# Kernel tuning notes

Measured on AMD Instinct MI355X. Metric: run time of the kernel, lower is better.

Reference implementation:

```python
import jax, jax.numpy as jnp
import numpy as np

B, S, PLM, G = 8, 2048, 768, 256
N_WM, E_WM = 50000, 800000
N_F, E_F = B * S, 131072
K = 4


def _gnn(h, src, dst, Ws, bs, n_nodes):
    # simple GCN-style message passing: aggregate neighbor features via
    # gather (h[src]) + scatter-add (segment_sum), then linear + relu.
    for W, b in zip(Ws, bs):
        m = jax.ops.segment_sum(h[src], dst, num_segments=n_nodes)  # [n, g]
        h = jax.nn.relu((h + m) @ W + b)
    return h


def setup_inputs() -> dict:
    key = jax.random.key(0)
    ks = jax.random.split(key, 16)
    std = 0.02
    inp = {
        "text_embeddings": jax.random.normal(ks[0], (B, S, PLM), jnp.float32),
        "wm_x": jax.random.normal(ks[1], (N_WM, G), jnp.float32),
        "wm_edge_index": jax.random.randint(ks[2], (2, E_WM), 0, N_WM),
        "token2nodepos": jax.random.randint(ks[3], (B * S, K), 0, N_WM),
        "fstm_node_ids": jax.random.randint(ks[4], (N_F,), 0, N_F),
        "fstm_edge_index": jax.random.randint(ks[5], (2, E_F), 0, N_F),
        # extra_emb: nn.Embedding(2, G, padding_idx=0) -> row 0 is zeros
        "extra_emb": jax.random.normal(ks[6], (2, G), jnp.float32).at[0].set(0.0) * std,
        "wm_W1": jax.random.normal(ks[7], (G, G), jnp.float32) * std,
        "wm_b1": jnp.zeros((G,), jnp.float32),
        "wm_W2": jax.random.normal(ks[8], (G, G), jnp.float32) * std,
        "wm_b2": jnp.zeros((G,), jnp.float32),
        "fstm_W1": jax.random.normal(ks[9], (G, G), jnp.float32) * std,
        "fstm_b1": jnp.zeros((G,), jnp.float32),
        "fstm_W2": jax.random.normal(ks[10], (G, G), jnp.float32) * std,
        "fstm_b2": jnp.zeros((G,), jnp.float32),
        "fc1_W": jax.random.normal(ks[11], (G + PLM, G), jnp.float32) * std,
        "fc1_b": jnp.zeros((G,), jnp.float32),
        "fc3_W": jax.random.normal(ks[12], (PLM + 2 * G, PLM), jnp.float32) * std,
        "fc3_b": jnp.zeros((PLM,), jnp.float32),
    }
    return inp


def reference(text_embeddings, wm_x, wm_edge_index, token2nodepos, fstm_node_ids,
              fstm_edge_index, extra_emb, wm_W1, wm_b1, wm_W2, wm_b2,
              fstm_W1, fstm_b1, fstm_W2, fstm_b2, fc1_W, fc1_b, fc3_W, fc3_b):
    # ====== WM ======
    graph_embeddings = _gnn(wm_x, wm_edge_index[0], wm_edge_index[1],
                            (wm_W1, wm_W2), (wm_b1, wm_b2), N_WM)  # [N_WM, G]
    table = jnp.concatenate([extra_emb, graph_embeddings], axis=0)  # [N_WM+2, G]
    # per-token gather-sum over K concept slots (original python loop, vectorized)
    tmp = jnp.sum(table[token2nodepos + 2], axis=1)  # [B*S, G]
    text_flat = text_embeddings.reshape(B * S, PLM)
    graph_text_embed = jnp.concatenate([tmp, text_flat], axis=-1) @ fc1_W + fc1_b  # [B*S, G]
    # ====== FSTM ======
    x = graph_text_embed[fstm_node_ids]  # [B*S, G]
    temporal = _gnn(x, fstm_edge_index[0], fstm_edge_index[1],
                    (fstm_W1, fstm_W2), (fstm_b1, fstm_b2), N_F)
    temporal = temporal.reshape(B, S, G)
    # ====== Final ======
    final_vec = jnp.concatenate(
        [text_embeddings, tmp.reshape(B, S, G), temporal], axis=-1)
    logits = final_vec @ fc3_W + fc3_b  # [B, S, PLM]
    return logits
```

## Files before the change

kernel.cpp:

```cpp
#include <hip/hip_runtime.h>

#define Bsz 8
#define Ssz 2048
#define PLM 768
#define Gd  256
#define N_WM 50000
#define E_WM 800000
#define N_F  16384
#define E_F  131072
#define Kc   4

typedef unsigned short ushort_t;
typedef short short8 __attribute__((ext_vector_type(8)));
typedef float f32x4 __attribute__((ext_vector_type(4)));

__device__ __forceinline__ ushort_t f2bf(float f) {
    union { float f; unsigned int u; } v; v.f = f;
    unsigned int r = (v.u + 0x7fffu + ((v.u >> 16) & 1u)) >> 16;
    return (ushort_t)r;
}
__device__ __forceinline__ float bf2f(ushort_t b) {
    union { unsigned int u; float f; } v; v.u = ((unsigned int)b) << 16;
    return v.f;
}
__device__ __forceinline__ float4 bf4f(ushort4 u) {
    return make_float4(bf2f(u.x), bf2f(u.y), bf2f(u.z), bf2f(u.w));
}

__device__ __forceinline__ void gl2lds16(const ushort_t* g, ushort_t* l) {
    __builtin_amdgcn_global_load_lds(
        (const __attribute__((address_space(1))) unsigned int*)g,
        (__attribute__((address_space(3))) unsigned int*)l, 16, 0, 0);
}

__device__ __forceinline__ void cvt4(const float* __restrict__ in,
                                     ushort_t* __restrict__ out, int i, int n4) {
    if (i < n4) {
        float4 v = ((const float4*)in)[i];
        ushort4 u;
        u.x = f2bf(v.x); u.y = f2bf(v.y); u.z = f2bf(v.z); u.w = f2bf(v.w);
        ((ushort4*)out)[i] = u;
    }
}
__device__ __forceinline__ void wtx(const float* __restrict__ W,
                                    ushort_t* __restrict__ Wt, int K, int N, int idx) {
    if (idx < N * K) {
        int n = idx / K, k = idx % K;
        Wt[idx] = f2bf(W[(size_t)k * N + n]);
    }
}

__global__ void conv_all(const float* __restrict__ wm_x, const float* __restrict__ text,
                         const float* __restrict__ extra,
                         const float* __restrict__ W1, const float* __restrict__ W2,
                         const float* __restrict__ W3, const float* __restrict__ W4,
                         const float* __restrict__ W5, const float* __restrict__ W6,
                         ushort_t* __restrict__ Xb, ushort_t* __restrict__ Tx,
                         ushort_t* __restrict__ Exb,
                         ushort_t* __restrict__ T1, ushort_t* __restrict__ T2,
                         ushort_t* __restrict__ T3, ushort_t* __restrict__ T4,
                         ushort_t* __restrict__ T5, ushort_t* __restrict__ T6) {
    int b = blockIdx.x, t = threadIdx.x;
    if (b < 12500) { cvt4(wm_x, Xb, b * 256 + t, 3200000); return; }
    b -= 12500;
    if (b < 12288) { cvt4(text, Tx, b * 256 + t, 3145728); return; }
    b -= 12288;
    if (b < 1) { cvt4(extra, Exb, t, 128); return; }
    b -= 1;
    if (b < 256) { wtx(W1, T1, 256, 256, b * 256 + t); return; }
    b -= 256;
    if (b < 256) { wtx(W2, T2, 256, 256, b * 256 + t); return; }
    b -= 256;
    if (b < 256) { wtx(W3, T3, 256, 256, b * 256 + t); return; }
    b -= 256;
    if (b < 256) { wtx(W4, T4, 256, 256, b * 256 + t); return; }
    b -= 256;
    if (b < 1024) { wtx(W5, T5, 1024, 256, b * 256 + t); return; }
    b -= 1024;
    wtx(W6, T6, 1280, 768, b * 256 + t);
}

#define WM_P 512
#define WM_CH 1563
#define WM_SHIFT 8
#define FS_P 128
#define FS_CH 1024
#define FS_SHIFT 6

__global__ __launch_bounds__(256) void csr_p1(const int* __restrict__ wm_dst,
                                              const int* __restrict__ f_dst,
                                              int* __restrict__ Cwm,
                                              int* __restrict__ Cfs) {
    __shared__ int hist[256];
    int b = blockIdx.x, t = threadIdx.x;
    hist[t] = 0; __syncthreads();
    if (b < WM_P) {
        int e0 = b * WM_CH, e1 = e0 + WM_CH; if (e1 > E_WM) e1 = E_WM;
        for (int e = e0 + t; e < e1; e += 256)
            atomicAdd(&hist[wm_dst[e] >> WM_SHIFT], 1);
        __syncthreads();
        Cwm[b * 256 + t] = hist[t];
    } else {
        int p = b - WM_P;
        int e0 = p * FS_CH, e1 = e0 + FS_CH;
        for (int e = e0 + t; e < e1; e += 256)
            atomicAdd(&hist[f_dst[e] >> FS_SHIFT], 1);
        __syncthreads();
        Cfs[p * 256 + t] = hist[t];
    }
}

__global__ __launch_bounds__(256) void csr_p2a(int* __restrict__ Cwm, int* __restrict__ BTwm,
                                               int* __restrict__ Cfs, int* __restrict__ BTfs) {
    __shared__ int sm[256];
    int b = blockIdx.x, t = threadIdx.x;
    int* C; int* BT; int P; int bk;
    if (b < 256) { C = Cwm; BT = BTwm; P = WM_P; bk = b; }
    else         { C = Cfs; BT = BTfs; P = FS_P; bk = b - 256; }
    int half = P >> 1;
    int v0 = 0, v1 = 0;
    if (t < half) { v0 = C[(2 * t) * 256 + bk]; v1 = C[(2 * t + 1) * 256 + bk]; }
    int s = v0 + v1;
    sm[t] = s; __syncthreads();
#pragma unroll
    for (int st = 1; st < 256; st <<= 1) {
        int x = (t >= st) ? sm[t - st] : 0;
        __syncthreads();
        sm[t] += x;
        __syncthreads();
    }
    int ex = sm[t] - s;
    if (t < half) {
        C[(2 * t) * 256 + bk] = ex;
        C[(2 * t + 1) * 256 + bk] = ex + v0;
    }
    if (t == 255) BT[bk] = sm[255];
}

__global__ __launch_bounds__(256) void csr_p2b(const int* __restrict__ BTwm,
                                               int* __restrict__ BSwm,
                                               const int* __restrict__ BTfs,
                                               int* __restrict__ BSfs) {
    __shared__ int sm[256];
    int t = threadIdx.x;
    const int* BT = blockIdx.x ? BTfs : BTwm;
    int* BS = blockIdx.x ? BSfs : BSwm;
    int E = blockIdx.x ? E_F : E_WM;
    int v = BT[t];
    sm[t] = v; __syncthreads();
#pragma unroll
    for (int st = 1; st < 256; st <<= 1) {
        int x = (t >= st) ? sm[t - st] : 0;
        __syncthreads();
        sm[t] += x;
        __syncthreads();
    }
    BS[t] = sm[t] - v;
    if (t == 255) BS[256] = E;
}

__global__ __launch_bounds__(256) void csr_p3(const int* __restrict__ wm_src,
                                              const int* __restrict__ wm_dst,
                                              const int* __restrict__ Cwm,
                                              const int* __restrict__ BSwm,
                                              int2* __restrict__ SEwm,
                                              const int* __restrict__ f_src,
                                              const int* __restrict__ f_dst,
                                              const int* __restrict__ Cfs,
                                              const int* __restrict__ BSfs,
                                              int2* __restrict__ SEfs) {
    __shared__ int cur[256];
    int b = blockIdx.x, t = threadIdx.x;
    if (b < WM_P) {
        cur[t] = Cwm[b * 256 + t] + BSwm[t];
        __syncthreads();
        int e0 = b * WM_CH, e1 = e0 + WM_CH; if (e1 > E_WM) e1 = E_WM;
        for (int e = e0 + t; e < e1; e += 256) {
            int d = wm_dst[e], s = wm_src[e];
            int pos = atomicAdd(&cur[d >> WM_SHIFT], 1);
            SEwm[pos] = make_int2(s, d);
        }
    } else {
        int p = b - WM_P;
        cur[t] = Cfs[p * 256 + t] + BSfs[t];
        __syncthreads();
        int e0 = p * FS_CH, e1 = e0 + FS_CH;
        for (int e = e0 + t; e < e1; e += 256) {
            int d = f_dst[e], s = f_src[e];
            int pos = atomicAdd(&cur[d >> FS_SHIFT], 1);
            SEfs[pos] = make_int2(s, d);
        }
    }
}

__global__ __launch_bounds__(256) void csr_p4(const int2* __restrict__ SEwm,
                                              const int* __restrict__ BSwm,
                                              int* __restrict__ wm_off,
                                              int* __restrict__ wm_bkt,
                                              const int2* __restrict__ SEfs,
                                              const int* __restrict__ BSfs,
                                              int* __restrict__ fs_off,
                                              int* __restrict__ fs_bkt) {
    __shared__ int cnt[256];
    __shared__ int sm[256];
    int ob = blockIdx.x, t = threadIdx.x;
    const int2* SE; const int* BS; int* off; int* bkt;
    int b, nb0, n, E, bw;
    if (ob < 256) { SE = SEwm; BS = BSwm; off = wm_off; bkt = wm_bkt;
                    b = ob; nb0 = b << WM_SHIFT; n = N_WM; E = E_WM; bw = 256; }
    else          { SE = SEfs; BS = BSfs; off = fs_off; bkt = fs_bkt;
                    b = ob - 256; nb0 = b << FS_SHIFT; n = N_F; E = E_F; bw = 64; }
    int e0 = BS[b], e1 = BS[b + 1];
    cnt[t] = 0; __syncthreads();
    for (int e = e0 + t; e < e1; e += 256)
        atomicAdd(&cnt[SE[e].y - nb0], 1);
    __syncthreads();
    int v = cnt[t];
    sm[t] = v; __syncthreads();
#pragma unroll
    for (int st = 1; st < 256; st <<= 1) {
        int x = (t >= st) ? sm[t - st] : 0;
        __syncthreads();
        sm[t] += x;
        __syncthreads();
    }
    int ex = sm[t] - v;
    if (t < bw && nb0 + t < n) off[nb0 + t] = e0 + ex;
    if (b == 0 && t == 0) off[n] = E;
    __syncthreads();
    cnt[t] = e0 + ex;
    __syncthreads();
    for (int e = e0 + t; e < e1; e += 256) {
        int2 sd = SE[e];
        int pos = atomicAdd(&cnt[sd.y - nb0], 1);
        bkt[pos] = sd.x;
    }
}

__global__ void aggregate_kernel(const ushort_t* __restrict__ h,
                                 const int* __restrict__ off,
                                 const int* __restrict__ bucket,
                                 ushort_t* __restrict__ hm, int n) {
    int i = blockIdx.x * 4 + (threadIdx.x >> 6);
    if (i >= n) return;
    int lane = threadIdx.x & 63;
    int s0 = off[i], s1 = off[i + 1];
    const ushort4* hp = (const ushort4*)h;
    float4 acc = bf4f(hp[(size_t)i * 64 + lane]);
    int j = s0;
    for (; j + 8 <= s1; j += 8) {
        int b0 = bucket[j + 0], b1 = bucket[j + 1];
        int b2 = bucket[j + 2], b3 = bucket[j + 3];
        int b4 = bucket[j + 4], b5 = bucket[j + 5];
        int b6 = bucket[j + 6], b7 = bucket[j + 7];
        ushort4 r0 = hp[(size_t)b0 * 64 + lane];
        ushort4 r1 = hp[(size_t)b1 * 64 + lane];
        ushort4 r2 = hp[(size_t)b2 * 64 + lane];
        ushort4 r3 = hp[(size_t)b3 * 64 + lane];
        ushort4 r4 = hp[(size_t)b4 * 64 + lane];
        ushort4 r5 = hp[(size_t)b5 * 64 + lane];
        ushort4 r6 = hp[(size_t)b6 * 64 + lane];
        ushort4 r7 = hp[(size_t)b7 * 64 + lane];
        float4 v0 = bf4f(r0), v1 = bf4f(r1), v2 = bf4f(r2), v3 = bf4f(r3);
        float4 v4 = bf4f(r4), v5 = bf4f(r5), v6 = bf4f(r6), v7 = bf4f(r7);
        acc.x += v0.x + v1.x + v2.x + v3.x + v4.x + v5.x + v6.x + v7.x;
        acc.y += v0.y + v1.y + v2.y + v3.y + v4.y + v5.y + v6.y + v7.y;
        acc.z += v0.z + v1.z + v2.z + v3.z + v4.z + v5.z + v6.z + v7.z;
        acc.w += v0.w + v1.w + v2.w + v3.w + v4.w + v5.w + v6.w + v7.w;
    }
    for (; j + 2 <= s1; j += 2) {
        int b0 = bucket[j + 0], b1 = bucket[j + 1];
        ushort4 r0 = hp[(size_t)b0 * 64 + lane];
        ushort4 r1 = hp[(size_t)b1 * 64 + lane];
        float4 v0 = bf4f(r0), v1 = bf4f(r1);
        acc.x += v0.x + v1.x; acc.y += v0.y + v1.y;
        acc.z += v0.z + v1.z; acc.w += v0.w + v1.w;
    }
    if (j < s1) {
        int b0 = bucket[j];
        float4 v0 = bf4f(hp[(size_t)b0 * 64 + lane]);
        acc.x += v0.x; acc.y += v0.y; acc.z += v0.z; acc.w += v0.w;
    }
    ushort4 u;
    u.x = f2bf(acc.x); u.y = f2bf(acc.y); u.z = f2bf(acc.z); u.w = f2bf(acc.w);
    ((ushort4*)hm)[(size_t)i * 64 + lane] = u;
}

__global__ void tmp_kernel(const ushort_t* __restrict__ gemb,
                           const ushort_t* __restrict__ extra,
                           const int* __restrict__ t2np,
                           ushort_t* __restrict__ D) {
    int i = blockIdx.x * 4 + (threadIdx.x >> 6);
    int lane = threadIdx.x & 63;
    float4 s = make_float4(0.f, 0.f, 0.f, 0.f);
#pragma unroll
    for (int k = 0; k < Kc; ++k) {
        int idx = t2np[i * Kc + k] + 2;
        const ushort4* row = (idx < 2) ? (const ushort4*)(extra + (size_t)idx * Gd)
                                       : (const ushort4*)(gemb + (size_t)(idx - 2) * Gd);
        float4 v = bf4f(row[lane]);
        s.x += v.x; s.y += v.y; s.z += v.z; s.w += v.w;
    }
    ushort4 u;
    u.x = f2bf(s.x); u.y = f2bf(s.y); u.z = f2bf(s.z); u.w = f2bf(s.w);
    ((ushort4*)D)[(size_t)i * 64 + lane] = u;
}

__global__ void gather_kernel(const ushort_t* __restrict__ Ein,
                              const int* __restrict__ ids,
                              ushort_t* __restrict__ F) {
    int i = blockIdx.x * 4 + (threadIdx.x >> 6);
    int lane = threadIdx.x & 63;
    ((ushort4*)F)[(size_t)i * 64 + lane] =
        ((const ushort4*)Ein)[(size_t)ids[i] * 64 + lane];
}

#define TBM 128
#define TBN 128
#define TBK 64

__device__ __forceinline__ void xcd_swizzle(int& bx, int& by) {
    int gx = gridDim.x;
    int nwg = gx * gridDim.y;
    int orig = by * gx + bx;
    int q = nwg >> 3, r = nwg & 7;
    int xcd = orig & 7, loc = orig >> 3;
    int wg = (xcd < r ? xcd * (q + 1) : r * (q + 1) + (xcd - r) * q) + loc;
    bx = wg % gx;
    by = wg / gx;
}

template <int MODE, int OUTBF>
__global__ __launch_bounds__(256) void mfma_gemm(
    const ushort_t* __restrict__ p0, const ushort_t* __restrict__ p1,
    const ushort_t* __restrict__ p2, const ushort_t* __restrict__ Wt,
    const float* __restrict__ bias, void* __restrict__ Cv,
    int M, int N, int K, int relu) {
    __shared__ ushort_t As[TBM * TBK];
    __shared__ ushort_t Bs[TBN * TBK];

    int tid  = threadIdx.x;
    int lane = tid & 63;
    int wave = tid >> 6;
    int wm = (wave >> 1) * 64, wn = (wave & 1) * 64;
    int bx = blockIdx.x, by = blockIdx.y;
    xcd_swizzle(bx, by);
    int row0 = by * TBM, col0 = bx * TBN;
    int l15 = lane & 15, l4 = lane >> 4;

    f32x4 acc[4][4];
#pragma unroll
    for (int i = 0; i < 4; ++i)
#pragma unroll
        for (int j = 0; j < 4; ++j)
            acc[i][j] = (f32x4){0.f, 0.f, 0.f, 0.f};

    for (int k0 = 0; k0 < K; k0 += TBK) {
#pragma unroll
        for (int it = 0; it < 4; ++it) {
            int eb = it * 2048 + wave * 512;
            int le = eb + lane * 8;
            int r  = le >> 6;
            int kl = le & 63;
            int grow = row0 + r; if (grow > M - 1) grow = M - 1;
            int gk = k0 + kl;
            const ushort_t* gp;
            if (MODE == 0)
                gp = p0 + (size_t)grow * K + gk;
            else if (MODE == 2)
                gp = (gk < 256) ? p0 + (size_t)grow * 256 + gk
                                : p1 + (size_t)grow * 768 + (gk - 256);
            else
                gp = (gk < 768) ? p0 + (size_t)grow * 768 + gk
                   : (gk < 1024) ? p1 + (size_t)grow * 256 + (gk - 768)
                                 : p2 + (size_t)grow * 256 + (gk - 1024);
            gl2lds16(gp, &As[eb]);
        }
#pragma unroll
        for (int it = 0; it < 4; ++it) {
            int eb = it * 2048 + wave * 512;
            int le = eb + lane * 8;
            int nl = le >> 6;
            int kl = le & 63;
            const ushort_t* gp = Wt + (size_t)(col0 + nl) * K + k0 + kl;
            gl2lds16(gp, &Bs[eb]);
        }
        __syncthreads();

#pragma unroll
        for (int ks = 0; ks < TBK; ks += 32) {
            short8 af[4], bfr[4];
#pragma unroll
            for (int mi = 0; mi < 4; ++mi)
                af[mi] = *(const short8*)&As[(wm + mi * 16 + l15) * TBK + ks + l4 * 8];
#pragma unroll
            for (int ni = 0; ni < 4; ++ni)
                bfr[ni] = *(const short8*)&Bs[(wn + ni * 16 + l15) * TBK + ks + l4 * 8];
#pragma unroll
            for (int mi = 0; mi < 4; ++mi)
#pragma unroll
                for (int ni = 0; ni < 4; ++ni)
                    acc[mi][ni] = __builtin_amdgcn_mfma_f32_16x16x32_bf16(
                        af[mi], bfr[ni], acc[mi][ni], 0, 0, 0);
        }
        __syncthreads();
    }

#pragma unroll
    for (int ni = 0; ni < 4; ++ni) {
        int c = col0 + wn + ni * 16 + l15;
        float bv = bias[c];
#pragma unroll
        for (int mi = 0; mi < 4; ++mi) {
#pragma unroll
            for (int r = 0; r < 4; ++r) {
                int rr = row0 + wm + mi * 16 + l4 * 4 + r;
                if (rr < M) {
                    float v = acc[mi][ni][r] + bv;
                    if (relu) v = fmaxf(v, 0.f);
                    if (OUTBF) ((ushort_t*)Cv)[(size_t)rr * N + c] = f2bf(v);
                    else       ((float*)Cv)[(size_t)rr * N + c] = v;
                }
            }
        }
    }
}

extern "C" void kernel_launch(void* const* d_in, const int* in_sizes, int n_in,
                              void* d_out, int out_size, void* d_ws, size_t ws_size,
                              hipStream_t stream) {
    const float* text    = (const float*)d_in[0];
    const float* wm_x    = (const float*)d_in[1];
    const int*   wm_ei   = (const int*)d_in[2];
    const int*   t2np    = (const int*)d_in[3];
    const int*   f_ids   = (const int*)d_in[4];
    const int*   f_ei    = (const int*)d_in[5];
    const float* extra   = (const float*)d_in[6];
    const float* wm_W1   = (const float*)d_in[7];
    const float* wm_b1   = (const float*)d_in[8];
    const float* wm_W2   = (const float*)d_in[9];
    const float* wm_b2   = (const float*)d_in[10];
    const float* fs_W1   = (const float*)d_in[11];
    const float* fs_b1   = (const float*)d_in[12];
    const float* fs_W2   = (const float*)d_in[13];
    const float* fs_b2   = (const float*)d_in[14];
    const float* fc1_W   = (const float*)d_in[15];
    const float* fc1_b   = (const float*)d_in[16];
    const float* fc3_W   = (const float*)d_in[17];
    const float* fc3_b   = (const float*)d_in[18];
    float* out = (float*)d_out;

    ushort_t* Xb  = (ushort_t*)d_ws;
    ushort_t* Ag  = Xb + 12800000;
    ushort_t* Gm  = Ag + 12800000;
    ushort_t* Tx  = Gm + 12800000;
    ushort_t* Dt  = Tx + 12582912;
    ushort_t* Ee  = Dt + 4194304;
    ushort_t* Wv  = Ee + 4194304;
    ushort_t* wt_wm1 = Wv;
    ushort_t* wt_wm2 = wt_wm1 + 65536;
    ushort_t* wt_fs1 = wt_wm2 + 65536;
    ushort_t* wt_fs2 = wt_fs1 + 65536;
    ushort_t* wt_fc1 = wt_fs2 + 65536;
    ushort_t* wt_fc3 = wt_fc1 + 262144;
    ushort_t* Exb    = wt_fc3 + 983040;
    int* wm_off = (int*)(Exb + 512);
    int* fs_off = wm_off + N_WM + 1;
    int* wm_bkt = fs_off + N_F + 1;
    int* fs_bkt = wm_bkt + E_WM;
    int2* SEwm = (int2*)Ag;
    int2* SEfs = SEwm + E_WM;
    int*  Cwm  = (int*)(SEfs + E_F);
    int*  Cfs  = Cwm + WM_P * 256;
    int*  BTwm = Cfs + FS_P * 256;
    int*  BTfs = BTwm + 256;
    int*  BSwm = BTfs + 256;
    int*  BSfs = BSwm + 257;

    ushort_t* h1 = Xb;
    ushort_t* F  = Gm;
    ushort_t* H  = Gm + 4194304;
    ushort_t* T  = Ee;

    const int* wm_src = wm_ei;
    const int* wm_dst = wm_ei + E_WM;
    const int* f_src  = f_ei;
    const int* f_dst  = f_ei + E_F;

    dim3 blk(256);
    dim3 gW(Gd / TBN, (N_WM + TBM - 1) / TBM);
    dim3 gF(Gd / TBN, N_F / TBM);
    dim3 gO(PLM / TBN, N_F / TBM);

    csr_p1<<<WM_P + FS_P, blk, 0, stream>>>(wm_dst, f_dst, Cwm, Cfs);
    csr_p2a<<<512, blk, 0, stream>>>(Cwm, BTwm, Cfs, BTfs);
    csr_p2b<<<2, blk, 0, stream>>>(BTwm, BSwm, BTfs, BSfs);
    csr_p3<<<WM_P + FS_P, blk, 0, stream>>>(wm_src, wm_dst, Cwm, BSwm, SEwm,
                                            f_src, f_dst, Cfs, BSfs, SEfs);
    csr_p4<<<512, blk, 0, stream>>>(SEwm, BSwm, wm_off, wm_bkt,
                                    SEfs, BSfs, fs_off, fs_bkt);

    conv_all<<<30677, blk, 0, stream>>>(wm_x, text, extra,
                                        wm_W1, wm_W2, fs_W1, fs_W2, fc1_W, fc3_W,
                                        Xb, Tx, Exb,
                                        wt_wm1, wt_wm2, wt_fs1, wt_fs2,
                                        wt_fc1, wt_fc3);

    aggregate_kernel<<<(N_WM + 3) / 4, blk, 0, stream>>>(Xb, wm_off, wm_bkt, Ag, N_WM);
    mfma_gemm<0, 1><<<gW, blk, 0, stream>>>(Ag, nullptr, nullptr, wt_wm1, wm_b1,
                                            h1, N_WM, Gd, Gd, 1);
    aggregate_kernel<<<(N_WM + 3) / 4, blk, 0, stream>>>(h1, wm_off, wm_bkt, Ag, N_WM);
    mfma_gemm<0, 1><<<gW, blk, 0, stream>>>(Ag, nullptr, nullptr, wt_wm2, wm_b2,
                                            Gm, N_WM, Gd, Gd, 1);
    tmp_kernel<<<N_F / 4, blk, 0, stream>>>(Gm, Exb, t2np, Dt);
    mfma_gemm<2, 1><<<gF, blk, 0, stream>>>(Dt, Tx, nullptr, wt_fc1, fc1_b,
                                            Ee, N_F, Gd, Gd + PLM, 0);
    gather_kernel<<<N_F / 4, blk, 0, stream>>>(Ee, f_ids, F);
    aggregate_kernel<<<N_F / 4, blk, 0, stream>>>(F, fs_off, fs_bkt, Ag, N_F);
    mfma_gemm<0, 1><<<gF, blk, 0, stream>>>(Ag, nullptr, nullptr, wt_fs1, fs_b1,
                                            H, N_F, Gd, Gd, 1);
    aggregate_kernel<<<N_F / 4, blk, 0, stream>>>(H, fs_off, fs_bkt, Ag, N_F);
    mfma_gemm<0, 1><<<gF, blk, 0, stream>>>(Ag, nullptr, nullptr, wt_fs2, fs_b2,
                                            T, N_F, Gd, Gd, 1);
    mfma_gemm<3, 0><<<gO, blk, 0, stream>>>(Tx, Dt, T, wt_fc3, fc3_b,
                                            out, N_F, PLM, PLM + 2 * Gd, 0);
}
```

Before: 556.0 us.

## Tile weight transposes via LDS, swizzle GEMM LDS, shrink tiles, deepen gather unroll

Weight transpose-and-convert now goes through a 64x64 shared-memory tile, so both the global reads and the writes are coalesced instead of strided. The GEMM is templated on block size and switches to 64x128 tiles, which doubles the number of blocks for the small-N GEMMs. It also XOR-swizzles the LDS column index to cut bank conflicts on fragment reads. The aggregation loop is unrolled to 16 independent gathers for more memory-level parallelism, at the cost of more registers and per-block reuse.

```diff
diff --git a/kernel.cpp b/kernel.cpp
--- a/kernel.cpp
+++ b/kernel.cpp
@@ -42,11 +42,26 @@
         ((ushort4*)out)[i] = u;
     }
 }
-__device__ __forceinline__ void wtx(const float* __restrict__ W,
-                                    ushort_t* __restrict__ Wt, int K, int N, int idx) {
-    if (idx < N * K) {
-        int n = idx / K, k = idx % K;
-        Wt[idx] = f2bf(W[(size_t)k * N + n]);
+
+__device__ __forceinline__ void wtx_tile(const float* __restrict__ W,
+                                         ushort_t* __restrict__ Wt,
+                                         int K, int N, int tile,
+                                         ushort_t (*sm)[65]) {
+    int kt = K >> 6;
+    int k0 = (tile % kt) << 6;
+    int n0 = (tile / kt) << 6;
+    int t = threadIdx.x;
+    int tr = t >> 6, tc = t & 63;
+#pragma unroll
+    for (int p = 0; p < 16; ++p) {
+        int k = p * 4 + tr;
+        sm[k][tc] = f2bf(W[(size_t)(k0 + k) * N + n0 + tc]);
+    }
+    __syncthreads();
+#pragma unroll
+    for (int p = 0; p < 16; ++p) {
+        int n = p * 4 + tr;
+        Wt[(size_t)(n0 + n) * K + k0 + tc] = sm[tc][n];
     }
 }
 
@@ -60,6 +75,7 @@
                          ushort_t* __restrict__ T1, ushort_t* __restrict__ T2,
                          ushort_t* __restrict__ T3, ushort_t* __restrict__ T4,
                          ushort_t* __restrict__ T5, ushort_t* __restrict__ T6) {
+    __shared__ ushort_t sm[64][65];
     int b = blockIdx.x, t = threadIdx.x;
     if (b < 12500) { cvt4(wm_x, Xb, b * 256 + t, 3200000); return; }
     b -= 12500;
@@ -67,17 +83,17 @@
     b -= 12288;
     if (b < 1) { cvt4(extra, Exb, t, 128); return; }
     b -= 1;
-    if (b < 256) { wtx(W1, T1, 256, 256, b * 256 + t); return; }
-    b -= 256;
-    if (b < 256) { wtx(W2, T2, 256, 256, b * 256 + t); return; }
-    b -= 256;
-    if (b < 256) { wtx(W3, T3, 256, 256, b * 256 + t); return; }
-    b -= 256;
-    if (b < 256) { wtx(W4, T4, 256, 256, b * 256 + t); return; }
-    b -= 256;
-    if (b < 1024) { wtx(W5, T5, 1024, 256, b * 256 + t); return; }
-    b -= 1024;
-    wtx(W6, T6, 1280, 768, b * 256 + t);
+    if (b < 16) { wtx_tile(W1, T1, 256, 256, b, sm); return; }
+    b -= 16;
+    if (b < 16) { wtx_tile(W2, T2, 256, 256, b, sm); return; }
+    b -= 16;
+    if (b < 16) { wtx_tile(W3, T3, 256, 256, b, sm); return; }
+    b -= 16;
+    if (b < 16) { wtx_tile(W4, T4, 256, 256, b, sm); return; }
+    b -= 16;
+    if (b < 64) { wtx_tile(W5, T5, 1024, 256, b, sm); return; }
+    b -= 64;
+    wtx_tile(W6, T6, 1280, 768, b, sm);
 }
 
 #define WM_P 512
@@ -248,38 +264,35 @@
     const ushort4* hp = (const ushort4*)h;
     float4 acc = bf4f(hp[(size_t)i * 64 + lane]);
     int j = s0;
-    for (; j + 8 <= s1; j += 8) {
-        int b0 = bucket[j + 0], b1 = bucket[j + 1];
-        int b2 = bucket[j + 2], b3 = bucket[j + 3];
-        int b4 = bucket[j + 4], b5 = bucket[j + 5];
-        int b6 = bucket[j + 6], b7 = bucket[j + 7];
-        ushort4 r0 = hp[(size_t)b0 * 64 + lane];
-        ushort4 r1 = hp[(size_t)b1 * 64 + lane];
-        ushort4 r2 = hp[(size_t)b2 * 64 + lane];
-        ushort4 r3 = hp[(size_t)b3 * 64 + lane];
-        ushort4 r4 = hp[(size_t)b4 * 64 + lane];
-        ushort4 r5 = hp[(size_t)b5 * 64 + lane];
-        ushort4 r6 = hp[(size_t)b6 * 64 + lane];
-        ushort4 r7 = hp[(size_t)b7 * 64 + lane];
-        float4 v0 = bf4f(r0), v1 = bf4f(r1), v2 = bf4f(r2), v3 = bf4f(r3);
-        float4 v4 = bf4f(r4), v5 = bf4f(r5), v6 = bf4f(r6), v7 = bf4f(r7);
-        acc.x += v0.x + v1.x + v2.x + v3.x + v4.x + v5.x + v6.x + v7.x;
-        acc.y += v0.y + v1.y + v2.y + v3.y + v4.y + v5.y + v6.y + v7.y;
-        acc.z += v0.z + v1.z + v2.z + v3.z + v4.z + v5.z + v6.z + v7.z;
-        acc.w += v0.w + v1.w + v2.w + v3.w + v4.w + v5.w + v6.w + v7.w;
-    }
-    for (; j + 2 <= s1; j += 2) {
-        int b0 = bucket[j + 0], b1 = bucket[j + 1];
-        ushort4 r0 = hp[(size_t)b0 * 64 + lane];
-        ushort4 r1 = hp[(size_t)b1 * 64 + lane];
-        float4 v0 = bf4f(r0), v1 = bf4f(r1);
-        acc.x += v0.x + v1.x; acc.y += v0.y + v1.y;
-        acc.z += v0.z + v1.z; acc.w += v0.w + v1.w;
-    }
-    if (j < s1) {
-        int b0 = bucket[j];
-        float4 v0 = bf4f(hp[(size_t)b0 * 64 + lane]);
-        acc.x += v0.x; acc.y += v0.y; acc.z += v0.z; acc.w += v0.w;
+    for (; j + 16 <= s1; j += 16) {
+        int bb[16];
+#pragma unroll
+        for (int q = 0; q < 16; ++q) bb[q] = bucket[j + q];
+        ushort4 rr[16];
+#pragma unroll
+        for (int q = 0; q < 16; ++q) rr[q] = hp[(size_t)bb[q] * 64 + lane];
+#pragma unroll
+        for (int q = 0; q < 16; ++q) {
+            float4 v = bf4f(rr[q]);
+            acc.x += v.x; acc.y += v.y; acc.z += v.z; acc.w += v.w;
+        }
+    }
+    for (; j + 4 <= s1; j += 4) {
+        int bb[4];
+#pragma unroll
+        for (int q = 0; q < 4; ++q) bb[q] = bucket[j + q];
+        ushort4 rr[4];
+#pragma unroll
+        for (int q = 0; q < 4; ++q) rr[q] = hp[(size_t)bb[q] * 64 + lane];
+#pragma unroll
+        for (int q = 0; q < 4; ++q) {
+            float4 v = bf4f(rr[q]);
+            acc.x += v.x; acc.y += v.y; acc.z += v.z; acc.w += v.w;
+        }
+    }
+    for (; j < s1; ++j) {
+        float4 v = bf4f(hp[(size_t)bucket[j] * 64 + lane]);
+        acc.x += v.x; acc.y += v.y; acc.z += v.z; acc.w += v.w;
     }
     ushort4 u;
     u.x = f2bf(acc.x); u.y = f2bf(acc.y); u.z = f2bf(acc.z); u.w = f2bf(acc.w);
@@ -315,9 +328,9 @@
         ((const ushort4*)Ein)[(size_t)ids[i] * 64 + lane];
 }
 
-#define TBM 128
-#define TBN 128
 #define TBK 64
+#define GBM 64
+#define GBN 128
 
 __device__ __forceinline__ void xcd_swizzle(int& bx, int& by) {
     int gx = gridDim.x;
@@ -330,38 +343,42 @@
     by = wg / gx;
 }
 
-template <int MODE, int OUTBF>
+template <int MODE, int OUTBF, int BM, int BN>
 __global__ __launch_bounds__(256) void mfma_gemm(
     const ushort_t* __restrict__ p0, const ushort_t* __restrict__ p1,
     const ushort_t* __restrict__ p2, const ushort_t* __restrict__ Wt,
     const float* __restrict__ bias, void* __restrict__ Cv,
     int M, int N, int K, int relu) {
-    __shared__ ushort_t As[TBM * TBK];
-    __shared__ ushort_t Bs[TBN * TBK];
+    constexpr int MR = BM / 32;
+    constexpr int NR = BN / 32;
+    constexpr int A_IT = (BM * TBK) / 2048;
+    constexpr int B_IT = (BN * TBK) / 2048;
+    __shared__ ushort_t As[BM * TBK];
+    __shared__ ushort_t Bs[BN * TBK];
 
     int tid  = threadIdx.x;
     int lane = tid & 63;
     int wave = tid >> 6;
-    int wm = (wave >> 1) * 64, wn = (wave & 1) * 64;
+    int wm = (wave >> 1) * (BM / 2), wn = (wave & 1) * (BN / 2);
     int bx = blockIdx.x, by = blockIdx.y;
     xcd_swizzle(bx, by);
-    int row0 = by * TBM, col0 = bx * TBN;
+    int row0 = by * BM, col0 = bx * BN;
     int l15 = lane & 15, l4 = lane >> 4;
 
-    f32x4 acc[4][4];
-#pragma unroll
-    for (int i = 0; i < 4; ++i)
-#pragma unroll
-        for (int j = 0; j < 4; ++j)
+    f32x4 acc[MR][NR];
+#pragma unroll
+    for (int i = 0; i < MR; ++i)
+#pragma unroll
+        for (int j = 0; j < NR; ++j)
             acc[i][j] = (f32x4){0.f, 0.f, 0.f, 0.f};
 
     for (int k0 = 0; k0 < K; k0 += TBK) {
 #pragma unroll
-        for (int it = 0; it < 4; ++it) {
+        for (int it = 0; it < A_IT; ++it) {
             int eb = it * 2048 + wave * 512;
             int le = eb + lane * 8;
             int r  = le >> 6;
-            int kl = le & 63;
+            int kl = (le ^ ((r & 7) << 3)) & 63;
             int grow = row0 + r; if (grow > M - 1) grow = M - 1;
             int gk = k0 + kl;
             const ushort_t* gp;
@@ -377,11 +394,11 @@
             gl2lds16(gp, &As[eb]);
         }
 #pragma unroll
-        for (int it = 0; it < 4; ++it) {
+        for (int it = 0; it < B_IT; ++it) {
             int eb = it * 2048 + wave * 512;
             int le = eb + lane * 8;
             int nl = le >> 6;
-            int kl = le & 63;
+            int kl = (le ^ ((nl & 7) << 3)) & 63;
             const ushort_t* gp = Wt + (size_t)(col0 + nl) * K + k0 + kl;
             gl2lds16(gp, &Bs[eb]);
         }
@@ -389,17 +406,23 @@
 
 #pragma unroll
         for (int ks = 0; ks < TBK; ks += 32) {
-            short8 af[4], bfr[4];
-#pragma unroll
-            for (int mi = 0; mi < 4; ++mi)
-                af[mi] = *(const short8*)&As[(wm + mi * 16 + l15) * TBK + ks + l4 * 8];
-#pragma unroll
-            for (int ni = 0; ni < 4; ++ni)
-                bfr[ni] = *(const short8*)&Bs[(wn + ni * 16 + l15) * TBK + ks + l4 * 8];
-#pragma unroll
-            for (int mi = 0; mi < 4; ++mi)
-#pragma unroll
-                for (int ni = 0; ni < 4; ++ni)
+            short8 af[MR], bfr[NR];
+#pragma unroll
+            for (int mi = 0; mi < MR; ++mi) {
+                int row = wm + mi * 16 + l15;
+                int col = (ks + l4 * 8) ^ ((row & 7) << 3);
+                af[mi] = *(const short8*)&As[row * TBK + col];
+            }
+#pragma unroll
+            for (int ni = 0; ni < NR; ++ni) {
+                int row = wn + ni * 16 + l15;
+                int col = (ks + l4 * 8) ^ ((row & 7) << 3);
+                bfr[ni] = *(const short8*)&Bs[row * TBK + col];
+            }
+#pragma unroll
+            for (int mi = 0; mi < MR; ++mi)
+#pragma unroll
+                for (int ni = 0; ni < NR; ++ni)
                     acc[mi][ni] = __builtin_amdgcn_mfma_f32_16x16x32_bf16(
                         af[mi], bfr[ni], acc[mi][ni], 0, 0, 0);
         }
@@ -407,11 +430,11 @@
     }
 
 #pragma unroll
-    for (int ni = 0; ni < 4; ++ni) {
+    for (int ni = 0; ni < NR; ++ni) {
         int c = col0 + wn + ni * 16 + l15;
         float bv = bias[c];
 #pragma unroll
-        for (int mi = 0; mi < 4; ++mi) {
+        for (int mi = 0; mi < MR; ++mi) {
 #pragma unroll
             for (int r = 0; r < 4; ++r) {
                 int rr = row0 + wm + mi * 16 + l4 * 4 + r;
@@ -488,9 +511,9 @@
     const int* f_dst  = f_ei + E_F;
 
     dim3 blk(256);
-    dim3 gW(Gd / TBN, (N_WM + TBM - 1) / TBM);
-    dim3 gF(Gd / TBN, N_F / TBM);
-    dim3 gO(PLM / TBN, N_F / TBM);
+    dim3 gW(Gd / GBN, (N_WM + GBM - 1) / GBM);
+    dim3 gF(Gd / GBN, N_F / GBM);
+    dim3 gO(PLM / GBN, N_F / GBM);
 
     csr_p1<<<WM_P + FS_P, blk, 0, stream>>>(wm_dst, f_dst, Cwm, Cfs);
     csr_p2a<<<512, blk, 0, stream>>>(Cwm, BTwm, Cfs, BTfs);
@@ -500,28 +523,28 @@
     csr_p4<<<512, blk, 0, stream>>>(SEwm, BSwm, wm_off, wm_bkt,
                                     SEfs, BSfs, fs_off, fs_bkt);
 
-    conv_all<<<30677, blk, 0, stream>>>(wm_x, text, extra,
+    conv_all<<<25157, blk, 0, stream>>>(wm_x, text, extra,
                                         wm_W1, wm_W2, fs_W1, fs_W2, fc1_W, fc3_W,
                                         Xb, Tx, Exb,
                                         wt_wm1, wt_wm2, wt_fs1, wt_fs2,
                                         wt_fc1, wt_fc3);
 
     aggregate_kernel<<<(N_WM + 3) / 4, blk, 0, stream>>>(Xb, wm_off, wm_bkt, Ag, N_WM);
-    mfma_gemm<0, 1><<<gW, blk, 0, stream>>>(Ag, nullptr, nullptr, wt_wm1, wm_b1,
-                                            h1, N_WM, Gd, Gd, 1);
+    mfma_gemm<0, 1, GBM, GBN><<<gW, blk, 0, stream>>>(Ag, nullptr, nullptr, wt_wm1,
+                                                      wm_b1, h1, N_WM, Gd, Gd, 1);
     aggregate_kernel<<<(N_WM + 3) / 4, blk, 0, stream>>>(h1, wm_off, wm_bkt, Ag, N_WM);
-    mfma_gemm<0, 1><<<gW, blk, 0, stream>>>(Ag, nullptr, nullptr, wt_wm2, wm_b2,
-                                            Gm, N_WM, Gd, Gd, 1);
+    mfma_gemm<0, 1, GBM, GBN><<<gW, blk, 0, stream>>>(Ag, nullptr, nullptr, wt_wm2,
+                                                      wm_b2, Gm, N_WM, Gd, Gd, 1);
     tmp_kernel<<<N_F / 4, blk, 0, stream>>>(Gm, Exb, t2np, Dt);
-    mfma_gemm<2, 1><<<gF, blk, 0, stream>>>(Dt, Tx, nullptr, wt_fc1, fc1_b,
-                                            Ee, N_F, Gd, Gd + PLM, 0);
+    mfma_gemm<2, 1, GBM, GBN><<<gF, blk, 0, stream>>>(Dt, Tx, nullptr, wt_fc1,
+                                                      fc1_b, Ee, N_F, Gd, Gd + PLM, 0);
     gather_kernel<<<N_F / 4, blk, 0, stream>>>(Ee, f_ids, F);
     aggregate_kernel<<<N_F / 4, blk, 0, stream>>>(F, fs_off, fs_bkt, Ag, N_F);
-    mfma_gemm<0, 1><<<gF, blk, 0, stream>>>(Ag, nullptr, nullptr, wt_fs1, fs_b1,
-                                            H, N_F, Gd, Gd, 1);
+    mfma_gemm<0, 1, GBM, GBN><<<gF, blk, 0, stream>>>(Ag, nullptr, nullptr, wt_fs1,
+                                                      fs_b1, H, N_F, Gd, Gd, 1);
     aggregate_kernel<<<N_F / 4, blk, 0, stream>>>(H, fs_off, fs_bkt, Ag, N_F);
-    mfma_gemm<0, 1><<<gF, blk, 0, stream>>>(Ag, nullptr, nullptr, wt_fs2, fs_b2,
-                                            T, N_F, Gd, Gd, 1);
-    mfma_gemm<3, 0><<<gO, blk, 0, stream>>>(Tx, Dt, T, wt_fc3, fc3_b,
-                                            out, N_F, PLM, PLM + 2 * Gd, 0);
-}
+    mfma_gemm<0, 1, GBM, GBN><<<gF, blk, 0, stream>>>(Ag, nullptr, nullptr, wt_fs2,
+                                                      fs_b2, T, N_F, Gd, Gd, 1);
+    mfma_gemm<3, 0, GBM, GBN><<<gO, blk, 0, stream>>>(Tx, Dt, T, wt_fc3, fc3_b,
+                                                      out, N_F, PLM, PLM + 2 * Gd, 0);
+}
```

New measurement: 533.5 us. -4.0%, faster.
